# Kernel optimization log

Measured on AMD Instinct MI355X. Metric: run time of the kernel, lower is better.

Reference implementation:

```python
import jax, jax.numpy as jnp
import numpy as np

B, N, C, E = 512, 128, 4, 300   # batch, context events, components per event, embed dim
V = 50000                       # event-arg vocab (padding row appended -> V+1)
H1, H2 = 512, 256               # arg_composition_layer_sizes
NF = 8                          # num_extracted_features
K = 11                          # KNRM kernel count

MUS = jnp.array([1.0, 0.9, 0.7, 0.5, 0.3, 0.1, -0.1, -0.3, -0.5, -0.7, -0.9], dtype=jnp.float32)
SIGMAS = jnp.array([1e-3] + [0.1] * 10, dtype=jnp.float32)


def setup_inputs() -> dict:
    key = jax.random.key(0)
    ks = jax.random.split(key, 16)
    s = 0.05
    inp = {
        "event_table": jax.random.normal(ks[0], (V + 1, E), jnp.float32) * s,
        "W1": jax.random.normal(ks[1], (H1, C * E), jnp.float32) * s,
        "b1": jnp.zeros((H1,), jnp.float32),
        "W2": jax.random.normal(ks[2], (H2, H1), jnp.float32) * s,
        "b2": jnp.zeros((H2,), jnp.float32),
        "Wv": jax.random.normal(ks[3], (9, E), jnp.float32) * s,
        "bv": jnp.zeros((9,), jnp.float32),
        "Wc": jax.random.normal(ks[4], (1, NF + 9 + K), jnp.float32) * s,
        "bc": jnp.zeros((1,), jnp.float32),
        "batch_event": jax.random.randint(ks[5], (B, C), 0, V),
        "batch_features": jax.random.normal(ks[6], (B, NF), jnp.float32),
        "batch_distances": jax.random.uniform(ks[7], (B, 9), jnp.float32),
        "batch_context": jax.random.randint(ks[8], (B, N, C), 0, V),
        "batch_slots": jax.random.randint(ks[9], (B,), 0, C),
    }
    return inp


def _mlp(x, W1, b1, W2, b2):
    x = jax.nn.relu(x @ W1.T + b1)
    return jax.nn.relu(x @ W2.T + b2)


def _l2norm(x):
    n = jnp.linalg.norm(x, axis=-1, keepdims=True)
    return x / jnp.maximum(n, 1e-12)


def _kernel_pool(trans):
    # trans: [B, M, N] cosine similarities; RBF kernels over values, reduce N.
    k = jnp.exp(-(trans[..., None] - MUS) ** 2 / (2.0 * SIGMAS ** 2))  # [B,M,N,K]
    pooled = jnp.sum(k, axis=2)                                        # [B,M,K]
    return jnp.log(jnp.clip(pooled, 1e-10, None)) * 0.01


def reference(event_table, W1, b1, W2, b2, Wv, bv, Wc, bc,
              batch_event, batch_features, batch_distances, batch_context, batch_slots):
    # embedding lookups
    event_emb = event_table[batch_event]        # [B, C, E]
    context_emb = event_table[batch_context]    # [B, N, C, E]

    # distance encoding: event-dependent Gaussian kernels (predicate detached)
    predicates = jax.lax.stop_gradient(event_emb[:, 1, :])       # [B, E]
    variances = jax.nn.softplus(predicates @ Wv.T + bv)          # [B, 9]
    dist_emb = jnp.exp(-(batch_distances * batch_distances) / variances)
    extracted = jnp.concatenate([dist_emb, batch_features], axis=1)  # [B, 17]

    # event / context representations via shared arg-composition MLP
    event_repr = _mlp(event_emb.reshape(B, 1, C * E), W1, b1, W2, b2)      # [B,1,H2]
    context_repr = _mlp(context_emb.reshape(B, N, C * E), W1, b1, W2, b2)  # [B,N,H2]

    # cosine-similarity bmm + kernel pooling
    trans = jnp.einsum('bmd,bnd->bmn', _l2norm(event_repr), _l2norm(context_repr))  # [B,1,N]
    kp_mtx = _kernel_pool(trans)                                                    # [B,1,K]

    all_features = jnp.concatenate([extracted[:, None, :], kp_mtx], axis=-1)  # [B,1,17+K]
    scores = (all_features @ Wc.T + bc)[..., 0]                               # [B,1]
    return jax.nn.sigmoid(scores)
```

## Files before the change

kernel.cpp:

```cpp
#include <hip/hip_runtime.h>
#include <hip/hip_bf16.h>

#define B_    512
#define N_    128
#define E_    300
#define EP    320
#define CE    1200
#define KP1   1280
#define H1_   512
#define H2_   256
#define MT    66048
#define VP1   50001
#define NTT   (VP1 * 40)
#define NTW1  (H1_ * 160)
#define NTW2  (H2_ * H1_ / 8)

typedef __attribute__((ext_vector_type(8))) short bf16x8;
typedef __attribute__((ext_vector_type(4))) float f32x4;
typedef __attribute__((ext_vector_type(4))) unsigned short us4;
typedef __attribute__((ext_vector_type(8))) unsigned short us8;
typedef __attribute__((ext_vector_type(2))) long lx2;

static __device__ __forceinline__ unsigned short f2bf(float f) {
  unsigned int u = __float_as_uint(f);
  u += 0x7fffu + ((u >> 16) & 1u);
  return (unsigned short)(u >> 16);
}
static __device__ __forceinline__ float bf2f(unsigned short h) {
  return __uint_as_float(((unsigned int)h) << 16);
}
static __device__ __forceinline__ void gl16(const void* g, void* l) {
  __builtin_amdgcn_global_load_lds((const __attribute__((address_space(1))) unsigned int*)g,
                                   (__attribute__((address_space(3))) unsigned int*)l, 16, 0, 0);
}
static __device__ __forceinline__ unsigned long long pk8f8(
    float f0, float f1, float f2, float f3, float f4, float f5, float f6, float f7) {
  int lo = __builtin_amdgcn_cvt_pk_fp8_f32(f0, f1, 0, false);
  lo = __builtin_amdgcn_cvt_pk_fp8_f32(f2, f3, lo, true);
  int hi = __builtin_amdgcn_cvt_pk_fp8_f32(f4, f5, 0, false);
  hi = __builtin_amdgcn_cvt_pk_fp8_f32(f6, f7, hi, true);
  return ((unsigned long long)(unsigned int)hi << 32) | (unsigned int)lo;
}

static __device__ __forceinline__ unsigned long long pack_unit(const float* __restrict__ comp,
                                                               int e) {
  if (e < 296) {
    float4 a = *reinterpret_cast<const float4*>(comp + e);
    float4 b = *reinterpret_cast<const float4*>(comp + e + 4);
    return pk8f8(a.x, a.y, a.z, a.w, b.x, b.y, b.z, b.w);
  } else if (e == 296) {
    float4 a = *reinterpret_cast<const float4*>(comp + 296);
    return pk8f8(a.x, a.y, a.z, a.w, 0.f, 0.f, 0.f, 0.f);
  }
  return 0ULL;
}

__global__ __launch_bounds__(256) void convert_k(
    const float* __restrict__ table, const float* __restrict__ W1, const float* __restrict__ W2,
    unsigned char* __restrict__ tb8, unsigned char* __restrict__ W1f8,
    unsigned short* __restrict__ W2b) {
  int i = blockIdx.x * 256 + threadIdx.x;
  if (i < NTT) {
    int r = i / 40, j = i - r * 40;
    int s = j >> 3, p = j & 7;
    int e = s * 64 + ((p & 1) * 4 + (p >> 1)) * 8;
    unsigned long long o = pack_unit(table + (size_t)r * 300, e);
    *reinterpret_cast<unsigned long long*>(tb8 + (size_t)r * EP + j * 8) = o;
  } else if (i < NTT + NTW1) {
    int j = i - NTT;
    int r = j / 160, jj = j - r * 160;
    int t = jj >> 3, p = jj & 7;
    int k = t * 64 + ((p & 1) * 4 + (p >> 1)) * 8;
    int c = k / EP, e = k - c * EP;
    unsigned long long o = pack_unit(W1 + (size_t)r * CE + c * 300, e);
    *reinterpret_cast<unsigned long long*>(W1f8 + (size_t)r * KP1 + jj * 8) = o;
  } else if (i < NTT + NTW1 + NTW2) {
    int j = i - NTT - NTW1;
    float4 a = *reinterpret_cast<const float4*>(W2 + (size_t)j * 8);
    float4 b = *reinterpret_cast<const float4*>(W2 + (size_t)j * 8 + 4);
    us8 o;
    o[0]=f2bf(a.x); o[1]=f2bf(a.y); o[2]=f2bf(a.z); o[3]=f2bf(a.w);
    o[4]=f2bf(b.x); o[5]=f2bf(b.y); o[6]=f2bf(b.z); o[7]=f2bf(b.w);
    *reinterpret_cast<us8*>(W2b + (size_t)j * 8) = o;
  }
}

__global__ __launch_bounds__(256) void gemm1_k(
    const unsigned char* __restrict__ tb8, const unsigned char* __restrict__ W1f8,
    const float* __restrict__ b1, const int* __restrict__ bev, const int* __restrict__ bctx,
    unsigned short* __restrict__ H1buf) {
  __shared__ unsigned char As[3][128 * 64];
  __shared__ unsigned char Bs[3][128 * 64];

  const int tid  = threadIdx.x;
  const int lane = tid & 63;
  const int w    = tid >> 6;
  const int wr   = w >> 1, wc = w & 1;
  const int wgid = (blockIdx.x & 7) * 258 + (blockIdx.x >> 3);
  const int m0 = (wgid >> 2) * 128;
  const int n0 = (wgid & 3) * 128;
  const int fr = lane & 15, fg = lane >> 4;

  const int l16 = (tid & 3) ^ ((tid >> 3) & 3);
  int idx[2][4];
#pragma unroll
  for (int i = 0; i < 2; ++i) {
    int mrow = m0 + i * 64 + (tid >> 2);
    int bidx = mrow / 129, nidx = mrow - bidx * 129;
    const int* p = (nidx < 128) ? bctx + ((size_t)bidx * 128 + nidx) * 4
                                : bev + (size_t)bidx * 4;
#pragma unroll
    for (int c = 0; c < 4; ++c) idx[i][c] = p[c];
  }
  const unsigned char* bsrc0 = W1f8 + (size_t)(n0 + (tid >> 2)) * KP1 + l16 * 16;
  const unsigned char* bsrc1 = bsrc0 + (size_t)64 * KP1;
  const int p16f = fg ^ ((fr >> 1) & 3);

  f32x4 acc[4][4];
#pragma unroll
  for (int mi = 0; mi < 4; ++mi)
#pragma unroll
    for (int ni = 0; ni < 4; ++ni)
#pragma unroll
      for (int r = 0; r < 4; ++r) acc[mi][ni][r] = 0.f;

#define STAGE1(BUF, KT)                                                       \
  do {                                                                        \
    int c_ = (KT) / 5;                                                        \
    int e_ = ((KT) - c_ * 5) * 64 + l16 * 16;                                 \
    int id0 = (c_ == 0) ? idx[0][0] : (c_ == 1) ? idx[0][1]                   \
            : (c_ == 2) ? idx[0][2] : idx[0][3];                              \
    int id1 = (c_ == 0) ? idx[1][0] : (c_ == 1) ? idx[1][1]                   \
            : (c_ == 2) ? idx[1][2] : idx[1][3];                              \
    gl16(tb8 + (size_t)id0 * EP + e_, &As[BUF][w * 1024]);                    \
    gl16(tb8 + (size_t)id1 * EP + e_, &As[BUF][4096 + w * 1024]);             \
    gl16(bsrc0 + (size_t)(KT) * 64, &Bs[BUF][w * 1024]);                      \
    gl16(bsrc1 + (size_t)(KT) * 64, &Bs[BUF][4096 + w * 1024]);               \
  } while (0)

#define COMPUTE1(BUF)                                                         \
  do {                                                                        \
    lx2 af[4], bf[4];                                                         \
    _Pragma("unroll")                                                         \
    for (int mi = 0; mi < 4; ++mi)                                            \
      af[mi] = *reinterpret_cast<const lx2*>(                                 \
          &As[BUF][(wr * 64 + mi * 16 + fr) * 64 + p16f * 16]);               \
    _Pragma("unroll")                                                         \
    for (int ni = 0; ni < 4; ++ni)                                            \
      bf[ni] = *reinterpret_cast<const lx2*>(                                 \
          &Bs[BUF][(wc * 64 + ni * 16 + fr) * 64 + p16f * 16]);               \
    __builtin_amdgcn_s_setprio(1);                                            \
    _Pragma("unroll")                                                         \
    for (int mi = 0; mi < 4; ++mi)                                            \
      _Pragma("unroll")                                                       \
      for (int ni = 0; ni < 4; ++ni)                                          \
        acc[mi][ni] = __builtin_amdgcn_mfma_f32_16x16x32_fp8_fp8(             \
            af[mi][0], bf[ni][0], acc[mi][ni], 0, 0, 0);                      \
    _Pragma("unroll")                                                         \
    for (int mi = 0; mi < 4; ++mi)                                            \
      _Pragma("unroll")                                                       \
      for (int ni = 0; ni < 4; ++ni)                                          \
        acc[mi][ni] = __builtin_amdgcn_mfma_f32_16x16x32_fp8_fp8(             \
            af[mi][1], bf[ni][1], acc[mi][ni], 0, 0, 0);                      \
    __builtin_amdgcn_s_setprio(0);                                            \
  } while (0)

  STAGE1(0, 0);
  STAGE1(1, 1);
  int cur = 0, nx = 2;
  for (int t = 0; t < 19; ++t) {
    asm volatile("s_waitcnt vmcnt(4)" ::: "memory");
    __builtin_amdgcn_s_barrier();
    if (t + 2 < 20) STAGE1(nx, t + 2);
    COMPUTE1(cur);
    cur = (cur == 2) ? 0 : cur + 1;
    nx  = (nx  == 2) ? 0 : nx  + 1;
  }
  asm volatile("s_waitcnt vmcnt(0)" ::: "memory");
  __builtin_amdgcn_s_barrier();
  COMPUTE1(cur);
#undef STAGE1
#undef COMPUTE1

  float bb[4];
#pragma unroll
  for (int ni = 0; ni < 4; ++ni) bb[ni] = b1[n0 + wc * 64 + ni * 16 + fr];
#pragma unroll
  for (int mi = 0; mi < 4; ++mi)
#pragma unroll
    for (int ni = 0; ni < 4; ++ni)
#pragma unroll
      for (int r = 0; r < 4; ++r) {
        float v = fmaxf(acc[mi][ni][r] + bb[ni], 0.f);
        int row = m0 + wr * 64 + mi * 16 + fg * 4 + r;
        int col = n0 + wc * 64 + ni * 16 + fr;
        H1buf[(size_t)row * H1_ + col] = f2bf(v);
      }
}

__global__ __launch_bounds__(512) void gemm2_k(
    const unsigned short* __restrict__ H1buf, const unsigned short* __restrict__ W2b,
    const float* __restrict__ b2, unsigned short* __restrict__ RPR) {
  __shared__ unsigned short As[3][128 * 32];
  __shared__ unsigned short Bs[3][256 * 32];
  __shared__ float rpart[128][4];
  __shared__ float rinv[128];

  const int tid  = threadIdx.x;
  const int lane = tid & 63;
  const int w    = tid >> 6;
  const int wr   = w >> 2, wc = w & 3;
  const int m0   = blockIdx.x * 128;
  const int fr = lane & 15, fg = lane >> 4;

  const int l16 = (tid & 3) ^ ((tid >> 3) & 3);
  const unsigned short* asrc = H1buf + (size_t)(m0 + (tid >> 2)) * H1_ + l16 * 8;
  const unsigned short* bsrc = W2b + (size_t)(tid >> 2) * H1_ + l16 * 8;
  const int p16f = fg ^ ((fr >> 1) & 3);

  f32x4 acc[4][4];
#pragma unroll
  for (int mi = 0; mi < 4; ++mi)
#pragma unroll
    for (int ni = 0; ni < 4; ++ni)
#pragma unroll
      for (int r = 0; r < 4; ++r) acc[mi][ni][r] = 0.f;

#define STAGE2(BUF, KT)                                                       \
  do {                                                                        \
    gl16(asrc + (KT) * 32, &As[BUF][w * 512]);                                \
    gl16(bsrc + (KT) * 32, &Bs[BUF][w * 512]);                                \
    gl16(bsrc + 128 * H1_ + (KT) * 32, &Bs[BUF][4096 + w * 512]);             \
  } while (0)

#define COMPUTE2(BUF)                                                         \
  do {                                                                        \
    bf16x8 af[4], bfv[4];                                                     \
    _Pragma("unroll")                                                         \
    for (int mi = 0; mi < 4; ++mi)                                            \
      af[mi] = *reinterpret_cast<const bf16x8*>(                              \
          &As[BUF][(wr * 64 + mi * 16 + fr) * 32 + p16f * 8]);                \
    _Pragma("unroll")                                                         \
    for (int ni = 0; ni < 4; ++ni)                                            \
      bfv[ni] = *reinterpret_cast<const bf16x8*>(                             \
          &Bs[BUF][(wc * 64 + ni * 16 + fr) * 32 + p16f * 8]);                \
    __builtin_amdgcn_s_setprio(1);                                            \
    _Pragma("unroll")                                                         \
    for (int mi = 0; mi < 4; ++mi)                                            \
      _Pragma("unroll")                                                       \
      for (int ni = 0; ni < 4; ++ni)                                          \
        acc[mi][ni] = __builtin_amdgcn_mfma_f32_16x16x32_bf16(                \
            af[mi], bfv[ni], acc[mi][ni], 0, 0, 0);                           \
    __builtin_amdgcn_s_setprio(0);                                            \
  } while (0)

  STAGE2(0, 0);
  STAGE2(1, 1);
  int cur = 0, nx = 2;
  for (int t = 0; t < 15; ++t) {
    asm volatile("s_waitcnt vmcnt(3)" ::: "memory");
    __builtin_amdgcn_s_barrier();
    if (t + 2 < 16) STAGE2(nx, t + 2);
    COMPUTE2(cur);
    cur = (cur == 2) ? 0 : cur + 1;
    nx  = (nx  == 2) ? 0 : nx  + 1;
  }
  asm volatile("s_waitcnt vmcnt(0)" ::: "memory");
  __builtin_amdgcn_s_barrier();
  COMPUTE2(cur);
#undef STAGE2
#undef COMPUTE2

  float bb[4];
#pragma unroll
  for (int ni = 0; ni < 4; ++ni) bb[ni] = b2[wc * 64 + ni * 16 + fr];
#pragma unroll
  for (int mi = 0; mi < 4; ++mi)
#pragma unroll
    for (int ni = 0; ni < 4; ++ni)
#pragma unroll
      for (int r = 0; r < 4; ++r)
        acc[mi][ni][r] = fmaxf(acc[mi][ni][r] + bb[ni], 0.f);

#pragma unroll
  for (int mi = 0; mi < 4; ++mi)
#pragma unroll
    for (int r = 0; r < 4; ++r) {
      float s = 0.f;
#pragma unroll
      for (int ni = 0; ni < 4; ++ni) s += acc[mi][ni][r] * acc[mi][ni][r];
      s += __shfl_xor(s, 1); s += __shfl_xor(s, 2);
      s += __shfl_xor(s, 4); s += __shfl_xor(s, 8);
      if (fr == 0) rpart[wr * 64 + mi * 16 + fg * 4 + r][wc] = s;
    }
  __syncthreads();
  if (tid < 128) {
    float s = rpart[tid][0] + rpart[tid][1] + rpart[tid][2] + rpart[tid][3];
    rinv[tid] = 1.f / fmaxf(sqrtf(s), 1e-12f);
  }
  __syncthreads();

#pragma unroll
  for (int mi = 0; mi < 4; ++mi)
#pragma unroll
    for (int r = 0; r < 4; ++r) {
      int lrow = wr * 64 + mi * 16 + fg * 4 + r;
      float sc = rinv[lrow];
#pragma unroll
      for (int ni = 0; ni < 4; ++ni) {
        int col = wc * 64 + ni * 16 + fr;
        RPR[(size_t)(m0 + lrow) * H2_ + col] = f2bf(acc[mi][ni][r] * sc);
      }
    }
}

__global__ __launch_bounds__(256) void final_k(
    const float* __restrict__ table, const float* __restrict__ Wv, const float* __restrict__ bv,
    const float* __restrict__ Wc, const float* __restrict__ bc, const int* __restrict__ bev,
    const float* __restrict__ bdist, const float* __restrict__ bfeat,
    const unsigned short* __restrict__ RPR, float* __restrict__ out) {
  const int b = blockIdx.x, tid = threadIdx.x, lane = tid & 63, w = tid >> 6;
  __shared__ float pred[E_];
  __shared__ float tarr[128];
  __shared__ float var_s[9];
  __shared__ float pool_s[2][11];

  const float MU[11]  = {1.0f, 0.9f, 0.7f, 0.5f, 0.3f, 0.1f, -0.1f, -0.3f, -0.5f, -0.7f, -0.9f};
  const float IS2[11] = {500000.f, 50.f, 50.f, 50.f, 50.f, 50.f, 50.f, 50.f, 50.f, 50.f, 50.f};

  const int prow = bev[b * 4 + 1];
  for (int e = tid; e < E_; e += 256) pred[e] = table[(size_t)prow * E_ + e];
  __syncthreads();

  if (tid < 144) {
    int j = tid >> 4, l = tid & 15;
    float s = 0.f;
    for (int e = l; e < E_; e += 16) s += pred[e] * Wv[j * E_ + e];
    s += __shfl_xor(s, 1); s += __shfl_xor(s, 2);
    s += __shfl_xor(s, 4); s += __shfl_xor(s, 8);
    if (l == 0) {
      float x = s + bv[j];
      var_s[j] = fmaxf(x, 0.f) + log1pf(expf(-fabsf(x)));
    }
  }

  const unsigned short* evp = RPR + ((size_t)b * 129 + 128) * H2_;
  us4 e4 = *reinterpret_cast<const us4*>(evp + lane * 4);
  const float e0 = bf2f(e4[0]), e1 = bf2f(e4[1]), e2 = bf2f(e4[2]), e3 = bf2f(e4[3]);
  for (int k = 0; k < 32; ++k) {
    int n = w * 32 + k;
    const unsigned short* cp = RPR + ((size_t)b * 129 + n) * H2_;
    us4 c4 = *reinterpret_cast<const us4*>(cp + lane * 4);
    float d = e0 * bf2f(c4[0]) + e1 * bf2f(c4[1]) + e2 * bf2f(c4[2]) + e3 * bf2f(c4[3]);
#pragma unroll
    for (int off = 32; off; off >>= 1) d += __shfl_xor(d, off);
    if (lane == 0) tarr[n] = d;
  }
  __syncthreads();

  if (tid < 128) {
    float t = tarr[tid];
    float kv[11];
#pragma unroll
    for (int kk = 0; kk < 11; ++kk) {
      float u = t - MU[kk];
      kv[kk] = expf(-u * u * IS2[kk]);
    }
#pragma unroll
    for (int off = 32; off; off >>= 1)
#pragma unroll
      for (int kk = 0; kk < 11; ++kk) kv[kk] += __shfl_xor(kv[kk], off);
    if (lane == 0)
#pragma unroll
      for (int kk = 0; kk < 11; ++kk) pool_s[w][kk] = kv[kk];
  }
  __syncthreads();

  if (tid == 0) {
    float score = bc[0];
    for (int j = 0; j < 9; ++j) {
      float d = bdist[b * 9 + j];
      score += Wc[j] * expf(-(d * d) / var_s[j]);
    }
    for (int i = 0; i < 8; ++i) score += Wc[9 + i] * bfeat[b * 8 + i];
    for (int kk = 0; kk < 11; ++kk) {
      float p = fmaxf(pool_s[0][kk] + pool_s[1][kk], 1e-10f);
      score += Wc[17 + kk] * (0.01f * logf(p));
    }
    out[b] = 1.f / (1.f + expf(-score));
  }
}

extern "C" void kernel_launch(void* const* d_in, const int* in_sizes, int n_in,
                              void* d_out, int out_size, void* d_ws, size_t ws_size,
                              hipStream_t stream) {
  const float* table = (const float*)d_in[0];
  const float* W1    = (const float*)d_in[1];
  const float* b1    = (const float*)d_in[2];
  const float* W2    = (const float*)d_in[3];
  const float* b2    = (const float*)d_in[4];
  const float* Wv    = (const float*)d_in[5];
  const float* bv    = (const float*)d_in[6];
  const float* Wc    = (const float*)d_in[7];
  const float* bc    = (const float*)d_in[8];
  const int*   bev   = (const int*)d_in[9];
  const float* bfeat = (const float*)d_in[10];
  const float* bdist = (const float*)d_in[11];
  const int*   bctx  = (const int*)d_in[12];
  float* out = (float*)d_out;

  auto align64 = [](size_t x) { return (x + 63) & ~(size_t)63; };
  size_t off = 0;
  size_t o_tb8  = off; off += align64((size_t)VP1 * EP);
  size_t o_W1f8 = off; off += align64((size_t)H1_ * KP1);
  size_t o_W2b  = off; off += align64((size_t)H2_ * H1_ * 2);
  size_t o_H1   = off; off += align64((size_t)MT * H1_ * 2);
  size_t o_RPR  = off; off += align64((size_t)MT * H2_ * 2);
  if (ws_size < off) {
    hipMemsetAsync(d_out, 0xBF, (size_t)out_size * 4, stream);
    return;
  }
  char* ws = (char*)d_ws;
  unsigned char*  tb8   = (unsigned char*)(ws + o_tb8);
  unsigned char*  W1f8  = (unsigned char*)(ws + o_W1f8);
  unsigned short* W2b   = (unsigned short*)(ws + o_W2b);
  unsigned short* H1buf = (unsigned short*)(ws + o_H1);
  unsigned short* RPR   = (unsigned short*)(ws + o_RPR);

  const int conv_items = NTT + NTW1 + NTW2;
  hipLaunchKernelGGL(convert_k, dim3((conv_items + 255) / 256), dim3(256), 0, stream,
                     table, W1, W2, tb8, W1f8, W2b);
  hipLaunchKernelGGL(gemm1_k, dim3(MT / 128 * 4), dim3(256), 0, stream,
                     tb8, W1f8, b1, bev, bctx, H1buf);
  hipLaunchKernelGGL(gemm2_k, dim3(MT / 128), dim3(512), 0, stream, H1buf, W2b, b2, RPR);
  hipLaunchKernelGGL(final_k, dim3(B_), dim3(256), 0, stream,
                     table, Wv, bv, Wc, bc, bev, bdist, bfeat, RPR, out);
}
```

Measured before the change: 154.1 us.

## Quantize hidden activations and W2 to FP8 for the second GEMM

Stores the first-layer activations as scaled FP8 in a permuted layout instead of bf16, and converts W2 to FP8 with the same interleaving. The second GEMM now uses fp8 MFMA with half the K iterations and rescales the accumulator before bias and ReLU. This halves the bytes written and read for the intermediate buffer and the loads in gemm2. In exchange it loses accuracy in the activations, relying on a fixed scale factor of 64.

```diff
diff --git a/kernel.cpp b/kernel.cpp
--- a/kernel.cpp
+++ b/kernel.cpp
@@ -13,7 +13,9 @@
 #define VP1   50001
 #define NTT   (VP1 * 40)
 #define NTW1  (H1_ * 160)
-#define NTW2  (H2_ * H1_ / 8)
+#define NTW2  (H2_ * 64)
+#define HSCL  64.f
+#define HINV  0.015625f
 
 typedef __attribute__((ext_vector_type(8))) short bf16x8;
 typedef __attribute__((ext_vector_type(4))) float f32x4;
@@ -58,7 +60,7 @@
 __global__ __launch_bounds__(256) void convert_k(
     const float* __restrict__ table, const float* __restrict__ W1, const float* __restrict__ W2,
     unsigned char* __restrict__ tb8, unsigned char* __restrict__ W1f8,
-    unsigned short* __restrict__ W2b) {
+    unsigned char* __restrict__ W2f8) {
   int i = blockIdx.x * 256 + threadIdx.x;
   if (i < NTT) {
     int r = i / 40, j = i - r * 40;
@@ -76,19 +78,21 @@
     *reinterpret_cast<unsigned long long*>(W1f8 + (size_t)r * KP1 + jj * 8) = o;
   } else if (i < NTT + NTW1 + NTW2) {
     int j = i - NTT - NTW1;
-    float4 a = *reinterpret_cast<const float4*>(W2 + (size_t)j * 8);
-    float4 b = *reinterpret_cast<const float4*>(W2 + (size_t)j * 8 + 4);
-    us8 o;
-    o[0]=f2bf(a.x); o[1]=f2bf(a.y); o[2]=f2bf(a.z); o[3]=f2bf(a.w);
-    o[4]=f2bf(b.x); o[5]=f2bf(b.y); o[6]=f2bf(b.z); o[7]=f2bf(b.w);
-    *reinterpret_cast<us8*>(W2b + (size_t)j * 8) = o;
+    int r = j >> 6, jj = j & 63;
+    int s = jj >> 3, p = jj & 7;
+    int e = s * 64 + ((p & 1) * 4 + (p >> 1)) * 8;
+    const float* src = W2 + (size_t)r * H1_ + e;
+    float4 a = *reinterpret_cast<const float4*>(src);
+    float4 b = *reinterpret_cast<const float4*>(src + 4);
+    unsigned long long o = pk8f8(a.x, a.y, a.z, a.w, b.x, b.y, b.z, b.w);
+    *reinterpret_cast<unsigned long long*>(W2f8 + (size_t)r * H1_ + jj * 8) = o;
   }
 }
 
 __global__ __launch_bounds__(256) void gemm1_k(
     const unsigned char* __restrict__ tb8, const unsigned char* __restrict__ W1f8,
     const float* __restrict__ b1, const int* __restrict__ bev, const int* __restrict__ bctx,
-    unsigned short* __restrict__ H1buf) {
+    unsigned char* __restrict__ H1f8) {
   __shared__ unsigned char As[3][128 * 64];
   __shared__ unsigned char Bs[3][128 * 64];
 
@@ -183,26 +187,32 @@
 #undef COMPUTE1
 
   float bb[4];
-#pragma unroll
-  for (int ni = 0; ni < 4; ++ni) bb[ni] = b1[n0 + wc * 64 + ni * 16 + fr];
+  int pos[4];
+  const int sbase = (n0 >> 6) + wc;
+#pragma unroll
+  for (int ni = 0; ni < 4; ++ni) {
+    bb[ni] = b1[n0 + wc * 64 + ni * 16 + fr];
+    int u = ni * 16 + fr;
+    pos[ni] = sbase * 64 + (((u >> 3) & 3) * 2 + (u >> 5)) * 8 + (u & 7);
+  }
 #pragma unroll
   for (int mi = 0; mi < 4; ++mi)
 #pragma unroll
     for (int ni = 0; ni < 4; ++ni)
 #pragma unroll
       for (int r = 0; r < 4; ++r) {
-        float v = fmaxf(acc[mi][ni][r] + bb[ni], 0.f);
+        float v = fmaxf(acc[mi][ni][r] + bb[ni], 0.f) * HSCL;
+        unsigned int pk = __builtin_amdgcn_cvt_pk_fp8_f32(v, v, 0, false);
         int row = m0 + wr * 64 + mi * 16 + fg * 4 + r;
-        int col = n0 + wc * 64 + ni * 16 + fr;
-        H1buf[(size_t)row * H1_ + col] = f2bf(v);
+        H1f8[(size_t)row * H1_ + pos[ni]] = (unsigned char)(pk & 0xFF);
       }
 }
 
 __global__ __launch_bounds__(512) void gemm2_k(
-    const unsigned short* __restrict__ H1buf, const unsigned short* __restrict__ W2b,
+    const unsigned char* __restrict__ H1f8, const unsigned char* __restrict__ W2f8,
     const float* __restrict__ b2, unsigned short* __restrict__ RPR) {
-  __shared__ unsigned short As[3][128 * 32];
-  __shared__ unsigned short Bs[3][256 * 32];
+  __shared__ unsigned char As[3][128 * 64];
+  __shared__ unsigned char Bs[3][256 * 64];
   __shared__ float rpart[128][4];
   __shared__ float rinv[128];
 
@@ -214,8 +224,8 @@
   const int fr = lane & 15, fg = lane >> 4;
 
   const int l16 = (tid & 3) ^ ((tid >> 3) & 3);
-  const unsigned short* asrc = H1buf + (size_t)(m0 + (tid >> 2)) * H1_ + l16 * 8;
-  const unsigned short* bsrc = W2b + (size_t)(tid >> 2) * H1_ + l16 * 8;
+  const unsigned char* asrc = H1f8 + (size_t)(m0 + (tid >> 2)) * H1_ + l16 * 16;
+  const unsigned char* bsrc = W2f8 + (size_t)(tid >> 2) * H1_ + l16 * 16;
   const int p16f = fg ^ ((fr >> 1) & 3);
 
   f32x4 acc[4][4];
@@ -228,39 +238,45 @@
 
 #define STAGE2(BUF, KT)                                                       \
   do {                                                                        \
-    gl16(asrc + (KT) * 32, &As[BUF][w * 512]);                                \
-    gl16(bsrc + (KT) * 32, &Bs[BUF][w * 512]);                                \
-    gl16(bsrc + 128 * H1_ + (KT) * 32, &Bs[BUF][4096 + w * 512]);             \
+    gl16(asrc + (KT) * 64, &As[BUF][w * 1024]);                               \
+    gl16(bsrc + (KT) * 64, &Bs[BUF][w * 1024]);                               \
+    gl16(bsrc + (size_t)128 * H1_ + (KT) * 64, &Bs[BUF][8192 + w * 1024]);    \
   } while (0)
 
 #define COMPUTE2(BUF)                                                         \
   do {                                                                        \
-    bf16x8 af[4], bfv[4];                                                     \
-    _Pragma("unroll")                                                         \
-    for (int mi = 0; mi < 4; ++mi)                                            \
-      af[mi] = *reinterpret_cast<const bf16x8*>(                              \
-          &As[BUF][(wr * 64 + mi * 16 + fr) * 32 + p16f * 8]);                \
+    lx2 af[4], bf[4];                                                         \
+    _Pragma("unroll")                                                         \
+    for (int mi = 0; mi < 4; ++mi)                                            \
+      af[mi] = *reinterpret_cast<const lx2*>(                                 \
+          &As[BUF][(wr * 64 + mi * 16 + fr) * 64 + p16f * 16]);               \
     _Pragma("unroll")                                                         \
     for (int ni = 0; ni < 4; ++ni)                                            \
-      bfv[ni] = *reinterpret_cast<const bf16x8*>(                             \
-          &Bs[BUF][(wc * 64 + ni * 16 + fr) * 32 + p16f * 8]);                \
+      bf[ni] = *reinterpret_cast<const lx2*>(                                 \
+          &Bs[BUF][(wc * 64 + ni * 16 + fr) * 64 + p16f * 16]);               \
     __builtin_amdgcn_s_setprio(1);                                            \
     _Pragma("unroll")                                                         \
     for (int mi = 0; mi < 4; ++mi)                                            \
       _Pragma("unroll")                                                       \
       for (int ni = 0; ni < 4; ++ni)                                          \
-        acc[mi][ni] = __builtin_amdgcn_mfma_f32_16x16x32_bf16(                \
-            af[mi], bfv[ni], acc[mi][ni], 0, 0, 0);                           \
+        acc[mi][ni] = __builtin_amdgcn_mfma_f32_16x16x32_fp8_fp8(             \
+            af[mi][0], bf[ni][0], acc[mi][ni], 0, 0, 0);                      \
+    _Pragma("unroll")                                                         \
+    for (int mi = 0; mi < 4; ++mi)                                            \
+      _Pragma("unroll")                                                       \
+      for (int ni = 0; ni < 4; ++ni)                                          \
+        acc[mi][ni] = __builtin_amdgcn_mfma_f32_16x16x32_fp8_fp8(             \
+            af[mi][1], bf[ni][1], acc[mi][ni], 0, 0, 0);                      \
     __builtin_amdgcn_s_setprio(0);                                            \
   } while (0)
 
   STAGE2(0, 0);
   STAGE2(1, 1);
   int cur = 0, nx = 2;
-  for (int t = 0; t < 15; ++t) {
+  for (int t = 0; t < 7; ++t) {
     asm volatile("s_waitcnt vmcnt(3)" ::: "memory");
     __builtin_amdgcn_s_barrier();
-    if (t + 2 < 16) STAGE2(nx, t + 2);
+    if (t + 2 < 8) STAGE2(nx, t + 2);
     COMPUTE2(cur);
     cur = (cur == 2) ? 0 : cur + 1;
     nx  = (nx  == 2) ? 0 : nx  + 1;
@@ -280,7 +296,7 @@
     for (int ni = 0; ni < 4; ++ni)
 #pragma unroll
       for (int r = 0; r < 4; ++r)
-        acc[mi][ni][r] = fmaxf(acc[mi][ni][r] + bb[ni], 0.f);
+        acc[mi][ni][r] = fmaxf(acc[mi][ni][r] * HINV + bb[ni], 0.f);
 
 #pragma unroll
   for (int mi = 0; mi < 4; ++mi)
@@ -413,8 +429,8 @@
   size_t off = 0;
   size_t o_tb8  = off; off += align64((size_t)VP1 * EP);
   size_t o_W1f8 = off; off += align64((size_t)H1_ * KP1);
-  size_t o_W2b  = off; off += align64((size_t)H2_ * H1_ * 2);
-  size_t o_H1   = off; off += align64((size_t)MT * H1_ * 2);
+  size_t o_W2f8 = off; off += align64((size_t)H2_ * H1_);
+  size_t o_H1   = off; off += align64((size_t)MT * H1_);
   size_t o_RPR  = off; off += align64((size_t)MT * H2_ * 2);
   if (ws_size < off) {
     hipMemsetAsync(d_out, 0xBF, (size_t)out_size * 4, stream);
@@ -423,16 +439,16 @@
   char* ws = (char*)d_ws;
   unsigned char*  tb8   = (unsigned char*)(ws + o_tb8);
   unsigned char*  W1f8  = (unsigned char*)(ws + o_W1f8);
-  unsigned short* W2b   = (unsigned short*)(ws + o_W2b);
-  unsigned short* H1buf = (unsigned short*)(ws + o_H1);
+  unsigned char*  W2f8  = (unsigned char*)(ws + o_W2f8);
+  unsigned char*  H1f8  = (unsigned char*)(ws + o_H1);
   unsigned short* RPR   = (unsigned short*)(ws + o_RPR);
 
   const int conv_items = NTT + NTW1 + NTW2;
   hipLaunchKernelGGL(convert_k, dim3((conv_items + 255) / 256), dim3(256), 0, stream,
-                     table, W1, W2, tb8, W1f8, W2b);
+                     table, W1, W2, tb8, W1f8, W2f8);
   hipLaunchKernelGGL(gemm1_k, dim3(MT / 128 * 4), dim3(256), 0, stream,
-                     tb8, W1f8, b1, bev, bctx, H1buf);
-  hipLaunchKernelGGL(gemm2_k, dim3(MT / 128), dim3(512), 0, stream, H1buf, W2b, b2, RPR);
+                     tb8, W1f8, b1, bev, bctx, H1f8);
+  hipLaunchKernelGGL(gemm2_k, dim3(MT / 128), dim3(512), 0, stream, H1f8, W2f8, b2, RPR);
   hipLaunchKernelGGL(final_k, dim3(B_), dim3(256), 0, stream,
                      table, Wv, bv, Wc, bc, bev, bdist, bfeat, RPR, out);
 }
```

Result: no change. 154.7 us (+0.4%).
